# Kernel optimization log

Measured on AMD Instinct MI355X. Metric: run time of the kernel, lower is better.

Reference implementation:

```python
import jax, jax.numpy as jnp
import numpy as np

N, L, S, E, H = 8, 4096, 4096, 256, 8
D = E // H
EPS = 1e-6


def setup_inputs() -> dict:
    key = jax.random.key(0)
    ks = jax.random.split(key, 12)
    sc = 1.0 / np.sqrt(E)
    return {
        "q": jax.random.normal(ks[0], (N, L, E), jnp.float32),
        "k": jax.random.normal(ks[1], (N, S, E), jnp.float32),
        "v": jax.random.normal(ks[2], (N, S, E), jnp.float32),
        "q_mask": jax.random.uniform(ks[3], (N, L)) > 0.2,
        "kv_mask": jax.random.uniform(ks[4], (N, S)) > 0.2,
        "Wq": jax.random.normal(ks[5], (E, E), jnp.float32) * sc,
        "bq": jax.random.normal(ks[6], (E,), jnp.float32) * sc,
        "Wk": jax.random.normal(ks[7], (E, E), jnp.float32) * sc,
        "bk": jax.random.normal(ks[8], (E,), jnp.float32) * sc,
        "Wv": jax.random.normal(ks[9], (E, E), jnp.float32) * sc,
        "bv": jax.random.normal(ks[10], (E,), jnp.float32) * sc,
        "Wm": jax.random.normal(ks[11], (E, E), jnp.float32) * sc,
    }


def reference(q, k, v, q_mask, kv_mask, Wq, bq, Wk, bk, Wv, bv, Wm):
    n, l, _ = q.shape
    s = k.shape[1]
    # QKV projections (torch Linear: x @ W.T + b), split into heads
    Q = (q @ Wq.T + bq).reshape(n, l, H, D)
    K = (k @ Wk.T + bk).reshape(n, s, H, D)
    V = (v @ Wv.T + bv).reshape(n, s, H, D)
    # elu feature map (elu(x) + 1)
    Qf = jax.nn.elu(Q) + 1.0
    Kf = jax.nn.elu(K) + 1.0
    qm = q_mask.astype(Qf.dtype)[:, :, None, None]
    km = kv_mask.astype(Kf.dtype)[:, :, None, None]
    Qf = Qf * qm
    Kf = Kf * km
    Vm = V * km / s  # values / v_length
    # KV aggregation: [n,h,d,v]
    KV = jnp.einsum('nshd,nshv->nhdv', Kf, Vm)
    # normalizer Z: [n,l,h]
    Z = 1.0 / (jnp.einsum('nlhd,nhd->nlh', Qf, Kf.sum(axis=1)) + EPS)
    out = jnp.einsum('nlhd,nhdv->nlhv', Qf, KV) * Z[..., None] * s
    # merge projection (no bias)
    return out.reshape(n, l, H * D) @ Wm.T
```

## Files before the change

### kernel.cpp

```cpp
#include <hip/hip_runtime.h>

#define EPSF 1e-6f

typedef __bf16 bf16;
typedef bf16 bf16x4 __attribute__((ext_vector_type(4)));
typedef bf16 bf16x8 __attribute__((ext_vector_type(8)));
typedef float f32x4 __attribute__((ext_vector_type(4)));
typedef unsigned int u32;


__device__ __forceinline__ void async_ld16(const void* g, void* l) {
    __builtin_amdgcn_global_load_lds(
        (const __attribute__((address_space(1))) u32*)g,
        (__attribute__((address_space(3))) u32*)l, 16, 0, 0);
}

__global__ __launch_bounds__(256) void wconv(
    const float* __restrict__ Wq, const float* __restrict__ Wk,
    const float* __restrict__ Wv, const float* __restrict__ Wm,
    bf16* __restrict__ Wb)
{
    const int b = blockIdx.x, t = threadIdx.x;
    const int m = b >> 6;
    const float* S = (m == 0) ? Wq : (m == 1) ? Wk : (m == 2) ? Wv : Wm;
    const int idx = (b & 63) * 1024 + t * 4;
    float4 v = *(const float4*)(S + idx);
    bf16x4 p = {(bf16)v.x, (bf16)v.y, (bf16)v.z, (bf16)v.w};
    *(bf16x4*)(Wb + (size_t)m * 65536 + idx) = p;
}

__global__ __launch_bounds__(256) void kvproj(
    const float* __restrict__ kin, const float* __restrict__ vin,
    const bf16* __restrict__ Wb,
    const float* __restrict__ bk, const float* __restrict__ bv,
    const int* __restrict__ kv_mask,
    float* __restrict__ part, float* __restrict__ part_ks)
{
    const int bx = blockIdx.x;
    const int j0 = bx * 128;
    const int n  = blockIdx.y >> 6;
    const int st = blockIdx.y & 63;
    const int s0 = st * 64;
    const size_t R0 = (size_t)n * 4096 + s0;

    const int t = threadIdx.x, lane = t & 63, w = t >> 6;
    const int ln15 = lane & 15, lg = lane >> 4;
    const int wn = w * 32;
    const int wbase = t & ~63;

    __shared__ __align__(16) char smem[36864];
    bf16*  Kf_ld = (bf16*)smem;
    float* Xs    = (float*)(smem + 18432);
    bf16*  Ws    = (bf16*)(smem + 18432 + 8192);
    bf16*  Vm_ld = (bf16*)(smem + 18432);

    float mv[4][4];
    #pragma unroll
    for (int mi = 0; mi < 4; ++mi)
        #pragma unroll
        for (int r = 0; r < 4; ++r)
            mv[mi][r] = kv_mask[R0 + mi * 16 + lg * 4 + r] ? 1.f : 0.f;

    #pragma unroll
    for (int z = 0; z < 2; ++z) {
        const float* X    = z ? vin : kin;
        const bf16*  W    = Wb + (size_t)(z + 1) * 65536;
        const float* bias = z ? bv : bk;
        bf16* Yt          = z ? Vm_ld : Kf_ld;

        f32x4 acc[4][2] = {};

        for (int k0 = 0; k0 < 256; k0 += 32) {
            #pragma unroll
            for (int i = 0; i < 2; ++i) {
                const int c = i * 256 + t, row = c >> 3, sc = c & 7;
                async_ld16(X + (R0 + row) * 256 + k0 + ((sc ^ (row & 7)) * 4),
                           Xs + (size_t)(i * 256 + wbase) * 4);
            }
            #pragma unroll
            for (int i = 0; i < 2; ++i) {
                const int c = i * 256 + t, g = c >> 3, c8 = c & 7;
                const int c8s = c8 ^ (g & 7);
                const int wrow = g * 2 + (c8s >> 2), gch = c8s & 3;
                async_ld16(W + (size_t)(j0 + wrow) * 256 + k0 + gch * 8,
                           Ws + (size_t)(i * 256 + wbase) * 8);
            }
            __syncthreads();

            bf16x8 a[4], b[2];
            #pragma unroll
            for (int mi = 0; mi < 4; ++mi) {
                const int r = mi * 16 + ln15, rb = r & 7;
                f32x4 x0 = *(const f32x4*)&Xs[r * 32 + (((lg * 2)     ^ rb) * 4)];
                f32x4 x1 = *(const f32x4*)&Xs[r * 32 + (((lg * 2 + 1) ^ rb) * 4)];
                a[mi] = bf16x8{(bf16)x0[0], (bf16)x0[1], (bf16)x0[2], (bf16)x0[3],
                               (bf16)x1[0], (bf16)x1[1], (bf16)x1[2], (bf16)x1[3]};
            }
            #pragma unroll
            for (int ni = 0; ni < 2; ++ni) {
                const int wr = wn + ni * 16 + ln15, g = wr >> 1;
                const int c8 = ((wr & 1) * 4 + lg) ^ (g & 7);
                b[ni] = *(const bf16x8*)&Ws[g * 64 + c8 * 8];
            }
            #pragma unroll
            for (int mi = 0; mi < 4; ++mi)
                #pragma unroll
                for (int ni = 0; ni < 2; ++ni)
                    acc[mi][ni] = __builtin_amdgcn_mfma_f32_16x16x32_bf16(
                        a[mi], b[ni], acc[mi][ni], 0, 0, 0);
            __syncthreads();
        }

        float bb[2];
        #pragma unroll
        for (int ni = 0; ni < 2; ++ni) bb[ni] = bias[j0 + wn + ni * 16 + ln15];
        #pragma unroll
        for (int ni = 0; ni < 2; ++ni) {
            const int col = wn + ni * 16 + ln15;
            #pragma unroll
            for (int mi = 0; mi < 4; ++mi) {
                const int rowb = mi * 16 + lg * 4;
                bf16x4 pk;
                #pragma unroll
                for (int r = 0; r < 4; ++r) {
                    float x = acc[mi][ni][r] + bb[ni];
                    if (z == 0) x = (x > 0.f) ? (x + 1.f) : __expf(x);
                    pk[r] = (bf16)(x * mv[mi][r]);
                }
                *(bf16x4*)&Yt[col * 72 + rowb] = pk;
            }
        }
        __syncthreads();
    }

    {
        const int c = t >> 1, sh = t & 1;
        const bf16* kp = Kf_ld + c * 72 + sh * 32;
        float s = 0.f;
        #pragma unroll
        for (int j = 0; j < 4; ++j) {
            bf16x8 vv = *(const bf16x8*)(kp + j * 8);
            #pragma unroll
            for (int jj = 0; jj < 8; ++jj) s += (float)vv[jj];
        }
        s += __shfl_xor(s, 1);
        if (sh == 0) part_ks[((size_t)(n * 64 + st)) * 256 + j0 + c] = s;
    }

    {
        const int cb = wn;
        f32x4 c2[2][2] = {};
        #pragma unroll
        for (int step = 0; step < 2; ++step) {
            const int sb = step * 32 + lg * 8;
            bf16x8 a[2], b[2];
            #pragma unroll
            for (int mi = 0; mi < 2; ++mi)
                a[mi] = *(const bf16x8*)&Kf_ld[(cb + mi * 16 + ln15) * 72 + sb];
            #pragma unroll
            for (int nj = 0; nj < 2; ++nj)
                b[nj] = *(const bf16x8*)&Vm_ld[(cb + nj * 16 + ln15) * 72 + sb];
            #pragma unroll
            for (int mi = 0; mi < 2; ++mi)
                #pragma unroll
                for (int nj = 0; nj < 2; ++nj)
                    c2[mi][nj] = __builtin_amdgcn_mfma_f32_16x16x32_bf16(
                        a[mi], b[nj], c2[mi][nj], 0, 0, 0);
        }
        float* kvh = part + ((size_t)((n * 64 + st) * 8) + bx * 4 + w) * 1024;
        #pragma unroll
        for (int mi = 0; mi < 2; ++mi)
            #pragma unroll
            for (int nj = 0; nj < 2; ++nj)
                *(f32x4*)&kvh[(nj * 16 + ln15) * 32 + mi * 16 + lg * 4] = c2[mi][nj];
    }
}

__global__ __launch_bounds__(256) void kv_reduce(
    const float* __restrict__ part, const float* __restrict__ part_ks,
    bf16* __restrict__ KVb, float* __restrict__ Ksum)
{
    const int nh = blockIdx.x, n = nh >> 3, h = nh & 7;
    const int t = threadIdx.x;
    f32x4 acc = {};
    const float* p = part + ((size_t)n * 512 + h) * 1024 + t * 4;
    for (int c = 0; c < 64; ++c)
        acc += *(const f32x4*)(p + (size_t)c * 8192);
    bf16x4 ob = {(bf16)acc[0], (bf16)acc[1], (bf16)acc[2], (bf16)acc[3]};
    *(bf16x4*)(KVb + (size_t)nh * 1024 + t * 4) = ob;
    if (t < 32) {
        float s = 0.f;
        const float* pk = part_ks + (size_t)n * 16384 + h * 32 + t;
        for (int c = 0; c < 64; ++c) s += pk[c * 256];
        Ksum[n * 256 + h * 32 + t] = s;
    }
}

__global__ __launch_bounds__(256) void attn(
    const float* __restrict__ qin, const bf16* __restrict__ Wb,
    const float* __restrict__ bq, const int* __restrict__ q_mask,
    const bf16* __restrict__ KVb, const float* __restrict__ Ksum,
    float* __restrict__ out)
{
    const int n = blockIdx.y, l0 = blockIdx.x * 64;
    const size_t R0 = (size_t)n * 4096 + l0;
    const int t = threadIdx.x, lane = t & 63, w = t >> 6;
    const int ln15 = lane & 15, lg = lane >> 4;
    const int wn = w * 64;
    const int wbase = t & ~63;

    const bf16* Wq = Wb;
    const bf16* Wm = Wb + 3 * 65536;

    __shared__ __align__(16) char smem[33792];
    float* Xs  = (float*)smem;
    bf16*  Wst = (bf16*)(smem + 8192);
    bf16 (*Qs)[264] = (bf16(*)[264])smem;
    __shared__ float KSs[256];
    __shared__ float Dens[64][9];

    KSs[t] = Ksum[n * 256 + t];

    {
        f32x4 acc[4][4] = {};
        for (int k0 = 0; k0 < 256; k0 += 32) {
            #pragma unroll
            for (int i = 0; i < 2; ++i) {
                const int c = i * 256 + t, row = c >> 3, sc = c & 7;
                async_ld16(qin + (R0 + row) * 256 + k0 + ((sc ^ (row & 7)) * 4),
                           Xs + (size_t)(i * 256 + wbase) * 4);
            }
            #pragma unroll
            for (int i = 0; i < 4; ++i) {
                const int c = i * 256 + t, g = c >> 3, c8 = c & 7;
                const int c8s = c8 ^ (g & 7);
                const int wrow = g * 2 + (c8s >> 2), gch = c8s & 3;
                async_ld16(Wq + (size_t)wrow * 256 + k0 + gch * 8,
                           Wst + (size_t)(i * 256 + wbase) * 8);
            }
            __syncthreads();

            bf16x8 a[4], b[4];
            #pragma unroll
            for (int mi = 0; mi < 4; ++mi) {
                const int r = mi * 16 + ln15, rb = r & 7;
                f32x4 x0 = *(const f32x4*)&Xs[r * 32 + (((lg * 2)     ^ rb) * 4)];
                f32x4 x1 = *(const f32x4*)&Xs[r * 32 + (((lg * 2 + 1) ^ rb) * 4)];
                a[mi] = bf16x8{(bf16)x0[0], (bf16)x0[1], (bf16)x0[2], (bf16)x0[3],
                               (bf16)x1[0], (bf16)x1[1], (bf16)x1[2], (bf16)x1[3]};
            }
            #pragma unroll
            for (int ni = 0; ni < 4; ++ni) {
                const int wr = wn + ni * 16 + ln15, g = wr >> 1;
                const int c8 = ((wr & 1) * 4 + lg) ^ (g & 7);
                b[ni] = *(const bf16x8*)&Wst[g * 64 + c8 * 8];
            }
            #pragma unroll
            for (int mi = 0; mi < 4; ++mi)
                #pragma unroll
                for (int ni = 0; ni < 4; ++ni)
                    acc[mi][ni] = __builtin_amdgcn_mfma_f32_16x16x32_bf16(
                        a[mi], b[ni], acc[mi][ni], 0, 0, 0);
            __syncthreads();
        }
        float bb[4];
        #pragma unroll
        for (int ni = 0; ni < 4; ++ni) bb[ni] = bq[wn + ni * 16 + ln15];
        float mv[4][4];
        #pragma unroll
        for (int mi = 0; mi < 4; ++mi)
            #pragma unroll
            for (int r = 0; r < 4; ++r)
                mv[mi][r] = q_mask[R0 + mi * 16 + lg * 4 + r] ? 1.f : 0.f;
        #pragma unroll
        for (int mi = 0; mi < 4; ++mi)
            #pragma unroll
            for (int r = 0; r < 4; ++r) {
                const int row = mi * 16 + lg * 4 + r;
                #pragma unroll
                for (int ni = 0; ni < 4; ++ni) {
                    float x = acc[mi][ni][r] + bb[ni];
                    x = (x > 0.f) ? (x + 1.f) : __expf(x);
                    Qs[row][wn + ni * 16 + ln15] = (bf16)(x * mv[mi][r]);
                }
            }
    }
    __syncthreads();

    #pragma unroll
    for (int i = 0; i < 2; ++i) {
        const int idx = t + i * 256;
        const int l = idx & 63, h = idx >> 6;
        float s = 0.f;
        #pragma unroll
        for (int d8 = 0; d8 < 4; ++d8) {
            bf16x8 qv = *(const bf16x8*)&Qs[l][h * 32 + d8 * 8];
            #pragma unroll
            for (int jj = 0; jj < 8; ++jj)
                s += (float)qv[jj] * KSs[h * 32 + d8 * 8 + jj];
        }
        Dens[l][h] = s;
    }
    __syncthreads();

    #pragma unroll
    for (int hh = 0; hh < 2; ++hh) {
        const int h = w * 2 + hh;
        const bf16* kvh = KVb + (size_t)(n * 8 + h) * 1024;
        bf16x8 a[2], b[4];
        #pragma unroll
        for (int mi = 0; mi < 2; ++mi)
            a[mi] = *(const bf16x8*)(kvh + (mi * 16 + ln15) * 32 + lg * 8);
        #pragma unroll
        for (int nj = 0; nj < 4; ++nj)
            b[nj] = *(const bf16x8*)&Qs[nj * 16 + ln15][h * 32 + lg * 8];
        f32x4 c[2][4];
        #pragma unroll
        for (int mi = 0; mi < 2; ++mi)
            #pragma unroll
            for (int nj = 0; nj < 4; ++nj) {
                f32x4 zz = {};
                c[mi][nj] = __builtin_amdgcn_mfma_f32_16x16x32_bf16(a[mi], b[nj], zz, 0, 0, 0);
            }
        #pragma unroll
        for (int nj = 0; nj < 4; ++nj) {
            const int l = nj * 16 + ln15;
            const float rcp = 1.f / (Dens[l][h] + EPSF);
            #pragma unroll
            for (int mi = 0; mi < 2; ++mi) {
                bf16x4 pk;
                #pragma unroll
                for (int r = 0; r < 4; ++r) pk[r] = (bf16)(c[mi][nj][r] * rcp);
                *(bf16x4*)&Qs[l][h * 32 + mi * 16 + lg * 4] = pk;
            }
        }
    }
    __syncthreads();

    {
        f32x4 acc[4][4] = {};
        #pragma unroll 2
        for (int k0 = 0; k0 < 256; k0 += 32) {
            bf16x8 a[4], b[4];
            #pragma unroll
            for (int mi = 0; mi < 4; ++mi)
                a[mi] = *(const bf16x8*)&Qs[mi * 16 + ln15][k0 + lg * 8];
            #pragma unroll
            for (int ni = 0; ni < 4; ++ni)
                b[ni] = *(const bf16x8*)(Wm + (size_t)(wn + ni * 16 + ln15) * 256 + k0 + lg * 8);
            #pragma unroll
            for (int mi = 0; mi < 4; ++mi)
                #pragma unroll
                for (int ni = 0; ni < 4; ++ni)
                    acc[mi][ni] = __builtin_amdgcn_mfma_f32_16x16x32_bf16(
                        a[mi], b[ni], acc[mi][ni], 0, 0, 0);
        }
        #pragma unroll
        for (int ni = 0; ni < 4; ++ni) {
            const int col = wn + ni * 16 + ln15;
            #pragma unroll
            for (int mi = 0; mi < 4; ++mi)
                #pragma unroll
                for (int r = 0; r < 4; ++r)
                    out[(R0 + mi * 16 + lg * 4 + r) * 256 + col] = acc[mi][ni][r];
        }
    }
}

extern "C" void kernel_launch(void* const* d_in, const int* in_sizes, int n_in,
                              void* d_out, int out_size, void* d_ws, size_t ws_size,
                              hipStream_t stream) {
    const float* q      = (const float*)d_in[0];
    const float* k      = (const float*)d_in[1];
    const float* v      = (const float*)d_in[2];
    const int*   q_mask = (const int*)  d_in[3];
    const int*   kv_mask= (const int*)  d_in[4];
    const float* Wq     = (const float*)d_in[5];
    const float* bq     = (const float*)d_in[6];
    const float* Wk     = (const float*)d_in[7];
    const float* bk     = (const float*)d_in[8];
    const float* Wv     = (const float*)d_in[9];
    const float* bv     = (const float*)d_in[10];
    const float* Wm     = (const float*)d_in[11];

    char* ws = (char*)d_ws;
    bf16*  Wb      = (bf16*)ws;
    float* part    = (float*)(ws + 524288);
    float* part_ks = (float*)(ws + 524288 + 16777216);
    bf16*  KVb     = (bf16*)(ws + 524288 + 16777216 + 524288);
    float* Ksum    = (float*)(ws + 524288 + 16777216 + 524288 + 131072);

    const dim3 blk(256);
    wconv    <<<dim3(256),    blk, 0, stream>>>(Wq, Wk, Wv, Wm, Wb);
    kvproj   <<<dim3(2, 512), blk, 0, stream>>>(k, v, Wb, bk, bv, kv_mask, part, part_ks);
    kv_reduce<<<dim3(64),     blk, 0, stream>>>(part, part_ks, KVb, Ksum);
    attn     <<<dim3(64, 8),  blk, 0, stream>>>(q, Wb, bq, q_mask, KVb, Ksum, (float*)d_out);
}
```

Baseline: 199.2 us.

## Double-buffer async global-to-LDS loads in projection GEMMs and widen kv_reduce grid

The K-loop of the kvproj and attn projection GEMMs now uses two LDS buffers. The next k-slice, and in kvproj the first V slice after the last K slice, is prefetched with async loads while the current slice feeds the MFMAs, and the trailing barrier of each iteration is removed. kv_reduce is split across four times as many blocks, each reducing a scalar per thread, so more CUs share the reduction. The cost is more LDS per block, which may lower occupancy, and an explicit vmcnt(0) drain at every iteration that limits how much load latency is actually hidden.

New measurement: 202.6 us. No clear change (+1.7%).

```diff
diff --git a/kernel.cpp b/kernel.cpp
--- a/kernel.cpp
+++ b/kernel.cpp
@@ -14,6 +14,8 @@
         (const __attribute__((address_space(1))) u32*)g,
         (__attribute__((address_space(3))) u32*)l, 16, 0, 0);
 }
+
+#define DRAIN_VM() asm volatile("s_waitcnt vmcnt(0)" ::: "memory")
 
 __global__ __launch_bounds__(256) void wconv(
     const float* __restrict__ Wq, const float* __restrict__ Wk,
@@ -48,11 +50,30 @@
     const int wn = w * 32;
     const int wbase = t & ~63;
 
-    __shared__ __align__(16) char smem[36864];
-    bf16*  Kf_ld = (bf16*)smem;
-    float* Xs    = (float*)(smem + 18432);
-    bf16*  Ws    = (bf16*)(smem + 18432 + 8192);
-    bf16*  Vm_ld = (bf16*)(smem + 18432);
+    __shared__ __align__(16) char smem[51200];
+    bf16* Kf_ld = (bf16*)smem;
+    bf16* Vm_ld = (bf16*)(smem + 18432);
+
+    auto STAGE = [&](int b, int zz, int k0) {
+        const float* X = zz ? vin : kin;
+        const bf16*  W = Wb + (size_t)(zz + 1) * 65536;
+        float* Xs = (float*)(smem + 18432 + b * 16384);
+        bf16*  Ws = (bf16*)(smem + 18432 + 8192 + b * 16384);
+        #pragma unroll
+        for (int i = 0; i < 2; ++i) {
+            const int c = i * 256 + t, row = c >> 3, sc = c & 7;
+            async_ld16(X + (R0 + row) * 256 + k0 + ((sc ^ (row & 7)) * 4),
+                       Xs + (size_t)(i * 256 + wbase) * 4);
+        }
+        #pragma unroll
+        for (int i = 0; i < 2; ++i) {
+            const int c = i * 256 + t, g = c >> 3, c8 = c & 7;
+            const int c8s = c8 ^ (g & 7);
+            const int wrow = g * 2 + (c8s >> 2), gch = c8s & 3;
+            async_ld16(W + (size_t)(j0 + wrow) * 256 + k0 + gch * 8,
+                       Ws + (size_t)(i * 256 + wbase) * 8);
+        }
+    };
 
     float mv[4][4];
     #pragma unroll
@@ -61,31 +82,25 @@
         for (int r = 0; r < 4; ++r)
             mv[mi][r] = kv_mask[R0 + mi * 16 + lg * 4 + r] ? 1.f : 0.f;
 
+    STAGE(0, 0, 0);
+
     #pragma unroll
     for (int z = 0; z < 2; ++z) {
-        const float* X    = z ? vin : kin;
-        const bf16*  W    = Wb + (size_t)(z + 1) * 65536;
         const float* bias = z ? bv : bk;
         bf16* Yt          = z ? Vm_ld : Kf_ld;
 
         f32x4 acc[4][2] = {};
 
-        for (int k0 = 0; k0 < 256; k0 += 32) {
-            #pragma unroll
-            for (int i = 0; i < 2; ++i) {
-                const int c = i * 256 + t, row = c >> 3, sc = c & 7;
-                async_ld16(X + (R0 + row) * 256 + k0 + ((sc ^ (row & 7)) * 4),
-                           Xs + (size_t)(i * 256 + wbase) * 4);
-            }
-            #pragma unroll
-            for (int i = 0; i < 2; ++i) {
-                const int c = i * 256 + t, g = c >> 3, c8 = c & 7;
-                const int c8s = c8 ^ (g & 7);
-                const int wrow = g * 2 + (c8s >> 2), gch = c8s & 3;
-                async_ld16(W + (size_t)(j0 + wrow) * 256 + k0 + gch * 8,
-                           Ws + (size_t)(i * 256 + wbase) * 8);
-            }
+        #pragma unroll 2
+        for (int t8 = 0; t8 < 8; ++t8) {
+            const int cur = t8 & 1;
+            DRAIN_VM();
             __syncthreads();
+            if (t8 < 7)      STAGE(cur ^ 1, z, (t8 + 1) * 32);
+            else if (z == 0) STAGE(cur ^ 1, 1, 0);
+
+            const float* Xs = (const float*)(smem + 18432 + cur * 16384);
+            const bf16*  Ws = (const bf16*)(smem + 18432 + 8192 + cur * 16384);
 
             bf16x8 a[4], b[2];
             #pragma unroll
@@ -108,8 +123,9 @@
                 for (int ni = 0; ni < 2; ++ni)
                     acc[mi][ni] = __builtin_amdgcn_mfma_f32_16x16x32_bf16(
                         a[mi], b[ni], acc[mi][ni], 0, 0, 0);
-            __syncthreads();
-        }
+        }
+
+        if (z == 1) { DRAIN_VM(); __syncthreads(); }
 
         float bb[2];
         #pragma unroll
@@ -130,8 +146,9 @@
                 *(bf16x4*)&Yt[col * 72 + rowb] = pk;
             }
         }
-        __syncthreads();
-    }
+    }
+    DRAIN_VM();
+    __syncthreads();
 
     {
         const int c = t >> 1, sh = t & 1;
@@ -180,15 +197,18 @@
     const float* __restrict__ part, const float* __restrict__ part_ks,
     bf16* __restrict__ KVb, float* __restrict__ Ksum)
 {
-    const int nh = blockIdx.x, n = nh >> 3, h = nh & 7;
+    const int b = blockIdx.x;
+    const int nh = b >> 2, q = b & 3;
+    const int n = nh >> 3, h = nh & 7;
     const int t = threadIdx.x;
-    f32x4 acc = {};
-    const float* p = part + ((size_t)n * 512 + h) * 1024 + t * 4;
+    const int off = q * 256 + t;
+    float acc = 0.f;
+    const float* p = part + ((size_t)n * 512 + h) * 1024 + off;
+    #pragma unroll 8
     for (int c = 0; c < 64; ++c)
-        acc += *(const f32x4*)(p + (size_t)c * 8192);
-    bf16x4 ob = {(bf16)acc[0], (bf16)acc[1], (bf16)acc[2], (bf16)acc[3]};
-    *(bf16x4*)(KVb + (size_t)nh * 1024 + t * 4) = ob;
-    if (t < 32) {
+        acc += p[(size_t)c * 8192];
+    KVb[(size_t)nh * 1024 + off] = (bf16)acc;
+    if (q == 0 && t < 32) {
         float s = 0.f;
         const float* pk = part_ks + (size_t)n * 16384 + h * 32 + t;
         for (int c = 0; c < 64; ++c) s += pk[c * 256];
@@ -212,33 +232,44 @@
     const bf16* Wq = Wb;
     const bf16* Wm = Wb + 3 * 65536;
 
-    __shared__ __align__(16) char smem[33792];
-    float* Xs  = (float*)smem;
-    bf16*  Wst = (bf16*)(smem + 8192);
+    __shared__ __align__(16) char smem[49152];
     bf16 (*Qs)[264] = (bf16(*)[264])smem;
     __shared__ float KSs[256];
     __shared__ float Dens[64][9];
 
+    auto STAGE = [&](int b, int k0) {
+        float* Xs  = (float*)(smem + b * 24576);
+        bf16*  Wst = (bf16*)(smem + b * 24576 + 8192);
+        #pragma unroll
+        for (int i = 0; i < 2; ++i) {
+            const int c = i * 256 + t, row = c >> 3, sc = c & 7;
+            async_ld16(qin + (R0 + row) * 256 + k0 + ((sc ^ (row & 7)) * 4),
+                       Xs + (size_t)(i * 256 + wbase) * 4);
+        }
+        #pragma unroll
+        for (int i = 0; i < 4; ++i) {
+            const int c = i * 256 + t, g = c >> 3, c8 = c & 7;
+            const int c8s = c8 ^ (g & 7);
+            const int wrow = g * 2 + (c8s >> 2), gch = c8s & 3;
+            async_ld16(Wq + (size_t)wrow * 256 + k0 + gch * 8,
+                       Wst + (size_t)(i * 256 + wbase) * 8);
+        }
+    };
+
+    STAGE(0, 0);
     KSs[t] = Ksum[n * 256 + t];
 
     {
         f32x4 acc[4][4] = {};
-        for (int k0 = 0; k0 < 256; k0 += 32) {
-            #pragma unroll
-            for (int i = 0; i < 2; ++i) {
-                const int c = i * 256 + t, row = c >> 3, sc = c & 7;
-                async_ld16(qin + (R0 + row) * 256 + k0 + ((sc ^ (row & 7)) * 4),
-                           Xs + (size_t)(i * 256 + wbase) * 4);
-            }
-            #pragma unroll
-            for (int i = 0; i < 4; ++i) {
-                const int c = i * 256 + t, g = c >> 3, c8 = c & 7;
-                const int c8s = c8 ^ (g & 7);
-                const int wrow = g * 2 + (c8s >> 2), gch = c8s & 3;
-                async_ld16(Wq + (size_t)wrow * 256 + k0 + gch * 8,
-                           Wst + (size_t)(i * 256 + wbase) * 8);
-            }
+        #pragma unroll 2
+        for (int t8 = 0; t8 < 8; ++t8) {
+            const int cur = t8 & 1;
+            DRAIN_VM();
             __syncthreads();
+            if (t8 < 7) STAGE(cur ^ 1, (t8 + 1) * 32);
+
+            const float* Xs  = (const float*)(smem + cur * 24576);
+            const bf16*  Wst = (const bf16*)(smem + cur * 24576 + 8192);
 
             bf16x8 a[4], b[4];
             #pragma unroll
@@ -261,8 +292,10 @@
                 for (int ni = 0; ni < 4; ++ni)
                     acc[mi][ni] = __builtin_amdgcn_mfma_f32_16x16x32_bf16(
                         a[mi], b[ni], acc[mi][ni], 0, 0, 0);
-            __syncthreads();
-        }
+        }
+        DRAIN_VM();
+        __syncthreads();
+
         float bb[4];
         #pragma unroll
         for (int ni = 0; ni < 4; ++ni) bb[ni] = bq[wn + ni * 16 + ln15];
@@ -393,6 +426,6 @@
     const dim3 blk(256);
     wconv    <<<dim3(256),    blk, 0, stream>>>(Wq, Wk, Wv, Wm, Wb);
     kvproj   <<<dim3(2, 512), blk, 0, stream>>>(k, v, Wb, bk, bv, kv_mask, part, part_ks);
-    kv_reduce<<<dim3(64),     blk, 0, stream>>>(part, part_ks, KVb, Ksum);
+    kv_reduce<<<dim3(256),    blk, 0, stream>>>(part, part_ks, KVb, Ksum);
     attn     <<<dim3(64, 8),  blk, 0, stream>>>(q, Wb, bq, q_mask, KVb, Ksum, (float*)d_out);
 }
```
